# Kernel tuning notes

Hardware: AMD Instinct MI355X
Metric: run time of the kernel (lower is better)

## Reference

```python
import jax, jax.numpy as jnp
import numpy as np

N_HEAD = 16

def setup_inputs() -> dict:
    key = jax.random.key(0)
    k1, k2, k3, k4 = jax.random.split(key, 4)
    B, S, D = 4, 1024, 1024
    x = jax.random.normal(k1, (B, S, D), dtype=jnp.float32)
    # 0/1 float mask: cls_mask[:,0] overrides row 0, cls_mask[:,1] overrides col 0
    cls_mask = jax.random.randint(k2, (B, 2, S), 0, 2).astype(jnp.float32)
    w_attn = jax.random.normal(k3, (D, 3 * D), dtype=jnp.float32) * 0.02
    b_attn = jnp.zeros((3 * D,), dtype=jnp.float32)
    w_proj = jax.random.normal(k4, (D, D), dtype=jnp.float32) * 0.02
    b_proj = jnp.zeros((D,), dtype=jnp.float32)
    return {"x": x, "cls_mask": cls_mask, "w_attn": w_attn, "b_attn": b_attn,
            "w_proj": w_proj, "b_proj": b_proj}

def reference(x, cls_mask, w_attn, b_attn, w_proj, b_proj):
    B, S, D = x.shape
    H = N_HEAD
    hd = D // H
    cm = jnp.broadcast_to(jnp.tril(jnp.ones((S, S), x.dtype))[None, None], (B, 1, S, S))
    cm = cm.at[:, :, 0, :].set(cls_mask[:, 0][:, None, :])
    cm = cm.at[:, :, :, 0].set(cls_mask[:, 1][:, None, :])
    qkv = x @ w_attn + b_attn                      # [B,S,3D]
    q, k, v = jnp.split(qkv, 3, axis=-1)
    split_heads = lambda t: t.reshape(B, S, H, hd).transpose(0, 2, 1, 3)  # [B,H,S,hd]
    q, k, v = split_heads(q), split_heads(k), split_heads(v)
    w = jnp.einsum('bhqd,bhkd->bhqk', q, k) / jnp.sqrt(jnp.asarray(hd, x.dtype))
    w = w * cm - 10000.0 * (1.0 - cm)
    w = jax.nn.softmax(w, axis=-1)
    a = jnp.einsum('bhqk,bhkd->bhqd', w, v)
    a = a.transpose(0, 2, 1, 3).reshape(B, S, D)   # merge heads
    a = a @ w_proj + b_proj
    present = jnp.stack((k, v))                    # [2,B,H,S,hd]
    return a, present
```

## Files before the change

kernel.cpp:

```cpp
#include <hip/hip_runtime.h>
#include <hip/hip_bf16.h>

typedef __bf16 bf16x8 __attribute__((ext_vector_type(8)));
typedef float f32x4 __attribute__((ext_vector_type(4)));

__device__ __forceinline__ f32x4 mfma16(bf16x8 a, bf16x8 b, f32x4 c) {
    return __builtin_amdgcn_mfma_f32_16x16x32_bf16(a, b, c, 0, 0, 0);
}

typedef __attribute__((address_space(1))) const unsigned int GUInt;
typedef __attribute__((address_space(3))) unsigned int LUInt;
__device__ __forceinline__ void gl_lds16(const void* g, void* l) {
    __builtin_amdgcn_global_load_lds((GUInt*)g, (LUInt*)l, 16, 0, 0);
}

__device__ __forceinline__ int psw(int row, int bir) {
    return row * 128 + (bir ^ ((row & 7) << 4));
}

__global__ __launch_bounds__(256) void prep_kernel(
    const float* __restrict__ x, __hip_bfloat16* __restrict__ Xbf,
    const float* __restrict__ w_attn, __hip_bfloat16* __restrict__ WattnT,
    const float* __restrict__ w_proj, __hip_bfloat16* __restrict__ WprojT) {
    __shared__ float tile[64][65];
    const int bid = blockIdx.x;
    const int tid = threadIdx.x;
    if (bid < 4096) {
        int i = bid * 256 + tid;
        float4 v = reinterpret_cast<const float4*>(x)[i];
        __hip_bfloat16 o[4];
        o[0] = __float2bfloat16(v.x); o[1] = __float2bfloat16(v.y);
        o[2] = __float2bfloat16(v.z); o[3] = __float2bfloat16(v.w);
        *reinterpret_cast<uint2*>(&Xbf[i * 4]) = *reinterpret_cast<const uint2*>(o);
        return;
    }
    const float* in; __hip_bfloat16* out; int K, N, t;
    if (bid < 4096 + 768) { t = bid - 4096; in = w_attn; out = WattnT; K = 1024; N = 3072; }
    else                  { t = bid - 4864; in = w_proj; out = WprojT; K = 1024; N = 1024; }
    const int kt = t & 15, nt = t >> 4;
    const int c = tid & 63, r4 = tid >> 6;
#pragma unroll
    for (int i = 0; i < 16; ++i) {
        int r = i * 4 + r4;
        tile[r][c] = in[(size_t)(kt * 64 + r) * N + nt * 64 + c];
    }
    __syncthreads();
#pragma unroll
    for (int i = 0; i < 16; ++i) {
        int rr = i * 4 + r4;
        out[(size_t)(nt * 64 + rr) * K + kt * 64 + c] = __float2bfloat16(tile[c][rr]);
    }
}

template <int EPI>
__global__ __launch_bounds__(256) void gemm_kernel(
    const __hip_bfloat16* __restrict__ A, const __hip_bfloat16* __restrict__ Bt,
    const float* __restrict__ bias, int M, int N, int K,
    float* __restrict__ Cf,
    __hip_bfloat16* __restrict__ Qbf, __hip_bfloat16* __restrict__ Kbf,
    __hip_bfloat16* __restrict__ VbfT, float* __restrict__ present) {
    __shared__ __align__(16) char As[128 * 128];
    __shared__ __align__(16) char Bs[128 * 128];
    const int tid = threadIdx.x;
    const int lane = tid & 63;
    const int w = tid >> 6;
    const int lr = lane & 15;
    const int lg = lane >> 4;
    const int wm = (w >> 1) * 64;
    const int wn = (w & 1) * 64;
    const int bm = blockIdx.y, bn = blockIdx.x;
    const int swz = (lr & 7) << 4;

    const int srow = tid >> 3;
    const int ccs = ((tid & 7) * 16) ^ ((srow & 7) << 4);
    const char* aBase = (const char*)A + ((size_t)(bm * 128 + srow) * K) * 2 + ccs;
    const char* bBase = (const char*)Bt + ((size_t)(bn * 128 + srow) * K) * 2 + ccs;

    f32x4 zv = {0.f, 0.f, 0.f, 0.f};
    f32x4 acc[4][4];
#pragma unroll
    for (int i = 0; i < 4; ++i)
#pragma unroll
        for (int j = 0; j < 4; ++j) acc[i][j] = zv;

    for (int k0 = 0; k0 < K; k0 += 64) {
#pragma unroll
        for (int j = 0; j < 4; ++j) {
            gl_lds16(aBase + ((size_t)j * 32 * K + k0) * 2, &As[j * 4096 + tid * 16]);
            gl_lds16(bBase + ((size_t)j * 32 * K + k0) * 2, &Bs[j * 4096 + tid * 16]);
        }
        __syncthreads();
#pragma unroll
        for (int kk = 0; kk < 2; ++kk) {
            bf16x8 af[4], bfr[4];
#pragma unroll
            for (int mt = 0; mt < 4; ++mt)
                af[mt] = *reinterpret_cast<const bf16x8*>(
                    &As[(wm + mt * 16 + lr) * 128 + ((kk * 64 + lg * 16) ^ swz)]);
#pragma unroll
            for (int nt = 0; nt < 4; ++nt)
                bfr[nt] = *reinterpret_cast<const bf16x8*>(
                    &Bs[(wn + nt * 16 + lr) * 128 + ((kk * 64 + lg * 16) ^ swz)]);
#pragma unroll
            for (int mt = 0; mt < 4; ++mt)
#pragma unroll
                for (int nt = 0; nt < 4; ++nt)
                    acc[mt][nt] = mfma16(af[mt], bfr[nt], acc[mt][nt]);
        }
        __syncthreads();
    }

#pragma unroll
    for (int mt = 0; mt < 4; ++mt) {
        const int mbase = bm * 128 + wm + mt * 16 + lg * 4;
        const int bb = mbase >> 10, s0 = mbase & 1023;
#pragma unroll
        for (int nt = 0; nt < 4; ++nt) {
            const int n = bn * 128 + wn + nt * 16 + lr;
            const float bias_n = bias[n];
            float v[4];
#pragma unroll
            for (int r = 0; r < 4; ++r) v[r] = acc[mt][nt][r] + bias_n;
            if (EPI == 0) {
#pragma unroll
                for (int r = 0; r < 4; ++r) Cf[(size_t)(mbase + r) * N + n] = v[r];
            } else {
                const int sec = n >> 10, nn = n & 1023;
                const int hh = nn >> 6, d = nn & 63;
                const int rowbase = ((bb * 16 + hh) * 1024 + s0) * 64 + d;
                if (sec == 0) {
#pragma unroll
                    for (int r = 0; r < 4; ++r) Qbf[rowbase + r * 64] = __float2bfloat16(v[r]);
                } else if (sec == 1) {
#pragma unroll
                    for (int r = 0; r < 4; ++r) {
                        Kbf[rowbase + r * 64] = __float2bfloat16(v[r]);
                        present[rowbase + r * 64] = v[r];
                    }
                } else {
                    __hip_bfloat16 pk[4];
#pragma unroll
                    for (int r = 0; r < 4; ++r) {
                        pk[r] = __float2bfloat16(v[r]);
                        present[4194304 + rowbase + r * 64] = v[r];
                    }
                    *reinterpret_cast<uint2*>(&VbfT[((bb * 16 + hh) * 64 + d) * 1024 + s0]) =
                        *reinterpret_cast<const uint2*>(pk);
                }
            }
        }
    }
}

template <bool FIRST>
__device__ __forceinline__ void attn_tile(
    const char* Kb, const char* Vb, int kv0, char* Pw,
    const bf16x8* aq, const float* clscol, const float* cls, int b, int qbase,
    f32x4* acc_o, f32x4& acc_l,
    int lr, int lg, int lk, int swz, bf16x8 ones, float SC) {
    f32x4 zv = {0.f, 0.f, 0.f, 0.f};
    f32x4 sacc[4];
#pragma unroll
    for (int nt = 0; nt < 4; ++nt) {
        const char* kr = Kb + (nt * 16 + lr) * 128;
        bf16x8 k0 = *reinterpret_cast<const bf16x8*>(kr + ((lg * 16) ^ swz));
        bf16x8 k1 = *reinterpret_cast<const bf16x8*>(kr + ((64 + lg * 16) ^ swz));
        sacc[nt] = mfma16(aq[1], k1, mfma16(aq[0], k0, zv));
    }
    float p[4][4];
#pragma unroll
    for (int nt = 0; nt < 4; ++nt) {
        int k_j = kv0 + nt * 16 + lr;
#pragma unroll
        for (int r = 0; r < 4; ++r) {
            int q_i = qbase + lg * 4 + r;
            float e = __builtin_amdgcn_exp2f(sacc[nt][r] * SC);
            p[nt][r] = (k_j <= q_i) ? e : 0.f;
        }
    }
    if (qbase == 0) {
#pragma unroll
        for (int nt = 0; nt < 4; ++nt) {
            float cr = cls[b * 2048 + kv0 + nt * 16 + lr];
            float e0 = __builtin_amdgcn_exp2f(sacc[nt][0] * SC);
            float pr = (cr != 0.f) ? e0 : 0.f;
            if (lg == 0) p[nt][0] = pr;
        }
    }
    if (FIRST) {
#pragma unroll
        for (int r = 0; r < 4; ++r) {
            float ec = __builtin_amdgcn_exp2f(sacc[0][r] * SC);
            float pc = (clscol[r] != 0.f) ? ec : 0.f;
            if (lr == 0) p[0][r] = pc;
        }
    }
#pragma unroll
    for (int nt = 0; nt < 4; ++nt)
#pragma unroll
        for (int r = 0; r < 4; ++r)
            *reinterpret_cast<__hip_bfloat16*>(&Pw[psw(lg * 4 + r, nt * 32 + lr * 2)]) =
                __float2bfloat16(p[nt][r]);
    bf16x8 pa0 = *reinterpret_cast<const bf16x8*>(&Pw[psw(lr, lk * 2)]);
    bf16x8 pa1 = *reinterpret_cast<const bf16x8*>(&Pw[psw(lr, 64 + lk * 2)]);
    acc_l = mfma16(pa1, ones, mfma16(pa0, ones, acc_l));
#pragma unroll
    for (int ntd = 0; ntd < 4; ++ntd) {
        const char* vr = Vb + (ntd * 16 + lr) * 128;
        bf16x8 v0 = *reinterpret_cast<const bf16x8*>(vr + ((lg * 16) ^ swz));
        bf16x8 v1 = *reinterpret_cast<const bf16x8*>(vr + ((64 + lg * 16) ^ swz));
        acc_o[ntd] = mfma16(pa1, v1, mfma16(pa0, v0, acc_o[ntd]));
    }
}

__global__ __launch_bounds__(256) void attn_kernel(
    const __hip_bfloat16* __restrict__ Qbf, const __hip_bfloat16* __restrict__ Kbf,
    const __hip_bfloat16* __restrict__ VbfT, const float* __restrict__ cls,
    __hip_bfloat16* __restrict__ Abf) {
    __shared__ __align__(16) char KV[2][16384];
    __shared__ __align__(16) char P_lds[4 * 2048];
    const int tid = threadIdx.x;
    const int lane = tid & 63;
    const int w = tid >> 6;
    const int lr = lane & 15;
    const int lg = lane >> 4;
    const int lk = lg * 8;
    const int qx = blockIdx.x, h = blockIdx.y, b = blockIdx.z;
    const int desc[16] = {15, 0, 14, 13, 12, 11, 10, 9, 8, 7, 6, 5, 4, 3, 2, 1};
    const int base = (qx + ((b & 2) ? 8 : 0)) & 15;
    const int pos = (b & 1) ? (15 - base) : base;
    const int qt = desc[pos];
    const int bh = b * 16 + h;
    const int qbase = qt * 64 + w * 16;
    char* Pw = &P_lds[w * 2048];
    const int ntiles = (qt == 0) ? 16 : (qt + 1);

    const char* kSrc = (const char*)Kbf + (size_t)bh * 131072;
    const char* vSrc = (const char*)VbfT + (size_t)bh * 131072;
    const int srow = tid >> 3;
    const int ccs = ((tid & 7) * 16) ^ ((srow & 7) << 4);

#define STAGE(BUF, T)                                                          \
    do {                                                                       \
        const int kv0s_ = (T) * 64;                                            \
        char* dst_ = &KV[BUF][tid * 16];                                       \
        gl_lds16(kSrc + (size_t)(kv0s_ + srow) * 128 + ccs, dst_);             \
        gl_lds16(kSrc + (size_t)(kv0s_ + 32 + srow) * 128 + ccs, dst_ + 4096); \
        gl_lds16(vSrc + (size_t)srow * 2048 + kv0s_ * 2 + ccs, dst_ + 8192);   \
        gl_lds16(vSrc + (size_t)(32 + srow) * 2048 + kv0s_ * 2 + ccs, dst_ + 12288); \
    } while (0)

    STAGE(0, 0);

    bf16x8 aq[2];
#pragma unroll
    for (int c = 0; c < 2; ++c)
        aq[c] = *reinterpret_cast<const bf16x8*>(&Qbf[(size_t)(bh * 1024 + qbase + lr) * 64 + c * 32 + lk]);

    float clscol[4];
#pragma unroll
    for (int r = 0; r < 4; ++r)
        clscol[r] = cls[b * 2048 + 1024 + qbase + lg * 4 + r];

    bf16x8 ones;
#pragma unroll
    for (int i = 0; i < 8; ++i) ones[i] = (__bf16)1.0f;

    const float SC = 0.125f * 1.44269504088896f;
    f32x4 zv = {0.f, 0.f, 0.f, 0.f};
    f32x4 acc_o[4];
    f32x4 acc_l = zv;
#pragma unroll
    for (int i = 0; i < 4; ++i) acc_o[i] = zv;

    const int swz = (lr & 7) << 4;
    __syncthreads();

    if (1 < ntiles) STAGE(1, 1);
    attn_tile<true>(KV[0], KV[0] + 8192, 0, Pw, aq, clscol, cls, b, qbase,
                    acc_o, acc_l, lr, lg, lk, swz, ones, SC);
    __syncthreads();
    for (int t = 1; t < ntiles; ++t) {
        const int buf = t & 1;
        if (t + 1 < ntiles) STAGE(buf ^ 1, t + 1);
        attn_tile<false>(KV[buf], KV[buf] + 8192, t * 64, Pw, aq, clscol, cls, b, qbase,
                         acc_o, acc_l, lr, lg, lk, swz, ones, SC);
        __syncthreads();
    }
#undef STAGE

#pragma unroll
    for (int r = 0; r < 4; ++r) {
        float inv = 1.f / acc_l[r];
        int q_i = qbase + lg * 4 + r;
#pragma unroll
        for (int ntd = 0; ntd < 4; ++ntd) {
            int dd = ntd * 16 + lr;
            Abf[(size_t)(b * 1024 + q_i) * 1024 + h * 64 + dd] = __float2bfloat16(acc_o[ntd][r] * inv);
        }
    }
}

extern "C" void kernel_launch(void* const* d_in, const int* in_sizes, int n_in,
                              void* d_out, int out_size, void* d_ws, size_t ws_size,
                              hipStream_t stream) {
    const float* x      = (const float*)d_in[0];
    const float* cls    = (const float*)d_in[1];
    const float* w_attn = (const float*)d_in[2];
    const float* b_attn = (const float*)d_in[3];
    const float* w_proj = (const float*)d_in[4];
    const float* b_proj = (const float*)d_in[5];
    float* out_a = (float*)d_out;
    float* present = out_a + 4194304;

    char* ws = (char*)d_ws;
    __hip_bfloat16* Xbf    = (__hip_bfloat16*)(ws);
    __hip_bfloat16* Abf    = (__hip_bfloat16*)(ws);
    __hip_bfloat16* WattnT = (__hip_bfloat16*)(ws + 12ull * 1024 * 1024);
    __hip_bfloat16* WprojT = (__hip_bfloat16*)(ws + 20ull * 1024 * 1024);
    __hip_bfloat16* Qbf    = (__hip_bfloat16*)(ws + 24ull * 1024 * 1024);
    __hip_bfloat16* Kbf    = (__hip_bfloat16*)(ws + 36ull * 1024 * 1024);
    __hip_bfloat16* VbfT   = (__hip_bfloat16*)(ws + 48ull * 1024 * 1024);

    prep_kernel<<<5120, 256, 0, stream>>>(x, Xbf, w_attn, WattnT, w_proj, WprojT);
    gemm_kernel<1><<<dim3(24, 32), 256, 0, stream>>>(Xbf, WattnT, b_attn, 4096, 3072, 1024,
                                                     nullptr, Qbf, Kbf, VbfT, present);
    attn_kernel<<<dim3(16, 16, 4), 256, 0, stream>>>(Qbf, Kbf, VbfT, cls, Abf);
    gemm_kernel<0><<<dim3(8, 32), 256, 0, stream>>>(Abf, WprojT, b_proj, 4096, 1024, 1024,
                                                    out_a, nullptr, nullptr, nullptr, nullptr);
}
```

Baseline: 108.4 us.

## Split CLS row into separate kernel and use 128-row attention blocks

Moves row 0's full-length CLS attention out of the main attention kernel into a small dedicated kernel. The q-tile holding row 0 previously had to scan all 16 KV tiles. With that gone, the main kernel switches to 512-thread blocks covering 128 query rows, with a simple mirrored ordering to balance the causal work, and each thread stages half as many loads. The cost is an extra kernel launch and a small, poorly parallel kernel over 64 (batch, head) pairs. The attention kernel's row-0 output is overwritten afterwards.

Result: slower. 114.3 us (+5.5%).

```diff
diff --git a/kernel.cpp b/kernel.cpp
--- a/kernel.cpp
+++ b/kernel.cpp
@@ -155,7 +155,7 @@
 template <bool FIRST>
 __device__ __forceinline__ void attn_tile(
     const char* Kb, const char* Vb, int kv0, char* Pw,
-    const bf16x8* aq, const float* clscol, const float* cls, int b, int qbase,
+    const bf16x8* aq, const float* clscol, int qbase,
     f32x4* acc_o, f32x4& acc_l,
     int lr, int lg, int lk, int swz, bf16x8 ones, float SC) {
     f32x4 zv = {0.f, 0.f, 0.f, 0.f};
@@ -176,15 +176,6 @@
             int q_i = qbase + lg * 4 + r;
             float e = __builtin_amdgcn_exp2f(sacc[nt][r] * SC);
             p[nt][r] = (k_j <= q_i) ? e : 0.f;
-        }
-    }
-    if (qbase == 0) {
-#pragma unroll
-        for (int nt = 0; nt < 4; ++nt) {
-            float cr = cls[b * 2048 + kv0 + nt * 16 + lr];
-            float e0 = __builtin_amdgcn_exp2f(sacc[nt][0] * SC);
-            float pr = (cr != 0.f) ? e0 : 0.f;
-            if (lg == 0) p[nt][0] = pr;
         }
     }
     if (FIRST) {
@@ -213,41 +204,36 @@
     }
 }
 
-__global__ __launch_bounds__(256) void attn_kernel(
+__global__ __launch_bounds__(512) void attn_kernel(
     const __hip_bfloat16* __restrict__ Qbf, const __hip_bfloat16* __restrict__ Kbf,
     const __hip_bfloat16* __restrict__ VbfT, const float* __restrict__ cls,
     __hip_bfloat16* __restrict__ Abf) {
     __shared__ __align__(16) char KV[2][16384];
-    __shared__ __align__(16) char P_lds[4 * 2048];
+    __shared__ __align__(16) char P_lds[8 * 2048];
     const int tid = threadIdx.x;
     const int lane = tid & 63;
     const int w = tid >> 6;
     const int lr = lane & 15;
     const int lg = lane >> 4;
     const int lk = lg * 8;
-    const int qx = blockIdx.x, h = blockIdx.y, b = blockIdx.z;
-    const int desc[16] = {15, 0, 14, 13, 12, 11, 10, 9, 8, 7, 6, 5, 4, 3, 2, 1};
-    const int base = (qx + ((b & 2) ? 8 : 0)) & 15;
-    const int pos = (b & 1) ? (15 - base) : base;
-    const int qt = desc[pos];
+    const int a = blockIdx.x, h = blockIdx.y, b = blockIdx.z;
+    const int a_eff = (b & 2) ? 7 - a : a;
     const int bh = b * 16 + h;
-    const int qbase = qt * 64 + w * 16;
+    const int qbase = a_eff * 128 + w * 16;
     char* Pw = &P_lds[w * 2048];
-    const int ntiles = (qt == 0) ? 16 : (qt + 1);
+    const int ntiles = 2 * a_eff + 2;
 
     const char* kSrc = (const char*)Kbf + (size_t)bh * 131072;
     const char* vSrc = (const char*)VbfT + (size_t)bh * 131072;
-    const int srow = tid >> 3;
-    const int ccs = ((tid & 7) * 16) ^ ((srow & 7) << 4);
+    const int sr = tid >> 3;
+    const int ccs = ((tid & 7) * 16) ^ ((sr & 7) << 4);
 
 #define STAGE(BUF, T)                                                          \
     do {                                                                       \
         const int kv0s_ = (T) * 64;                                            \
         char* dst_ = &KV[BUF][tid * 16];                                       \
-        gl_lds16(kSrc + (size_t)(kv0s_ + srow) * 128 + ccs, dst_);             \
-        gl_lds16(kSrc + (size_t)(kv0s_ + 32 + srow) * 128 + ccs, dst_ + 4096); \
-        gl_lds16(vSrc + (size_t)srow * 2048 + kv0s_ * 2 + ccs, dst_ + 8192);   \
-        gl_lds16(vSrc + (size_t)(32 + srow) * 2048 + kv0s_ * 2 + ccs, dst_ + 12288); \
+        gl_lds16(kSrc + (size_t)(kv0s_ + sr) * 128 + ccs, dst_);               \
+        gl_lds16(vSrc + (size_t)sr * 2048 + kv0s_ * 2 + ccs, dst_ + 8192);     \
     } while (0)
 
     STAGE(0, 0);
@@ -277,13 +263,13 @@
     __syncthreads();
 
     if (1 < ntiles) STAGE(1, 1);
-    attn_tile<true>(KV[0], KV[0] + 8192, 0, Pw, aq, clscol, cls, b, qbase,
+    attn_tile<true>(KV[0], KV[0] + 8192, 0, Pw, aq, clscol, qbase,
                     acc_o, acc_l, lr, lg, lk, swz, ones, SC);
     __syncthreads();
     for (int t = 1; t < ntiles; ++t) {
         const int buf = t & 1;
         if (t + 1 < ntiles) STAGE(buf ^ 1, t + 1);
-        attn_tile<false>(KV[buf], KV[buf] + 8192, t * 64, Pw, aq, clscol, cls, b, qbase,
+        attn_tile<false>(KV[buf], KV[buf] + 8192, t * 64, Pw, aq, clscol, qbase,
                          acc_o, acc_l, lr, lg, lk, swz, ones, SC);
         __syncthreads();
     }
@@ -298,6 +284,62 @@
             int dd = ntd * 16 + lr;
             Abf[(size_t)(b * 1024 + q_i) * 1024 + h * 64 + dd] = __float2bfloat16(acc_o[ntd][r] * inv);
         }
+    }
+}
+
+__global__ __launch_bounds__(256) void cls_row_kernel(
+    const __hip_bfloat16* __restrict__ Qbf, const __hip_bfloat16* __restrict__ Kbf,
+    const __hip_bfloat16* __restrict__ VbfT, const float* __restrict__ cls,
+    __hip_bfloat16* __restrict__ Abf) {
+    __shared__ float q_sh[64];
+    __shared__ float p_sh[1024];
+    __shared__ float l_sh[4];
+    __shared__ float o_sh[4][64];
+    const int h = blockIdx.x, b = blockIdx.y;
+    const int bh = b * 16 + h;
+    const int tid = threadIdx.x, w = tid >> 6, lane = tid & 63;
+    const float SC = 0.125f * 1.44269504088896f;
+
+    if (tid < 64) q_sh[tid] = __bfloat162float(Qbf[(size_t)bh * 65536 + tid]);
+    __syncthreads();
+
+    float lpart = 0.f;
+#pragma unroll
+    for (int jj = 0; jj < 4; ++jj) {
+        const int j = tid * 4 + jj;
+        const bf16x8* krow = reinterpret_cast<const bf16x8*>(&Kbf[(size_t)bh * 65536 + j * 64]);
+        float s = 0.f;
+#pragma unroll
+        for (int c = 0; c < 8; ++c) {
+            bf16x8 k8 = krow[c];
+#pragma unroll
+            for (int e = 0; e < 8; ++e) s += q_sh[c * 8 + e] * (float)k8[e];
+        }
+        bool keep = (cls[b * 2048 + j] != 0.f);
+        if (j == 0) keep = (cls[b * 2048 + 1024] != 0.f);
+        float pj = keep ? __builtin_amdgcn_exp2f(s * SC) : 0.f;
+        p_sh[j] = pj;
+        lpart += pj;
+    }
+#pragma unroll
+    for (int off = 32; off >= 1; off >>= 1) lpart += __shfl_xor(lpart, off);
+    if (lane == 0) l_sh[w] = lpart;
+    __syncthreads();
+    const float l = l_sh[0] + l_sh[1] + l_sh[2] + l_sh[3];
+
+    float od = 0.f;
+    const __hip_bfloat16* vrow = &VbfT[(size_t)bh * 65536 + (size_t)lane * 1024 + w * 256];
+#pragma unroll 8
+    for (int c = 0; c < 32; ++c) {
+        bf16x8 v8 = *reinterpret_cast<const bf16x8*>(&vrow[c * 8]);
+#pragma unroll
+        for (int e = 0; e < 8; ++e) od += p_sh[w * 256 + c * 8 + e] * (float)v8[e];
+    }
+    o_sh[w][lane] = od;
+    __syncthreads();
+    if (tid < 64) {
+        float o = (o_sh[0][tid] + o_sh[1][tid] + o_sh[2][tid] + o_sh[3][tid]) / l;
+        Abf[(size_t)b * 1048576 + h * 64 + tid] = __float2bfloat16(o);
     }
 }
 
@@ -325,7 +367,8 @@
     prep_kernel<<<5120, 256, 0, stream>>>(x, Xbf, w_attn, WattnT, w_proj, WprojT);
     gemm_kernel<1><<<dim3(24, 32), 256, 0, stream>>>(Xbf, WattnT, b_attn, 4096, 3072, 1024,
                                                      nullptr, Qbf, Kbf, VbfT, present);
-    attn_kernel<<<dim3(16, 16, 4), 256, 0, stream>>>(Qbf, Kbf, VbfT, cls, Abf);
+    attn_kernel<<<dim3(8, 16, 4), 512, 0, stream>>>(Qbf, Kbf, VbfT, cls, Abf);
+    cls_row_kernel<<<dim3(16, 4), 256, 0, stream>>>(Qbf, Kbf, VbfT, cls, Abf);
     gemm_kernel<0><<<dim3(8, 32), 256, 0, stream>>>(Abf, WprojT, b_proj, 4096, 1024, 1024,
                                                     out_a, nullptr, nullptr, nullptr, nullptr);
 }
```
